# Performance work log

Measured on AMD Instinct MI355X. Metric: run time of the kernel, lower is better.

The kernel has to match this reference:

```python
import jax, jax.numpy as jnp
import numpy as np

R = 2  # decimation factor


def _cheby1_sos(N=8, rp=0.05, Wn=1.0 / R):
    """Chebyshev type-I lowpass, second-order sections (matches scipy.signal.cheby1 math)."""
    eps = np.sqrt(10.0 ** (rp / 10.0) - 1.0)
    mu = np.arcsinh(1.0 / eps) / N
    k = np.arange(1, N + 1)
    theta = np.pi * (2 * k - 1) / (2 * N)
    # analog prototype poles (no zeros)
    p = -np.sinh(mu) * np.sin(theta) + 1j * np.cosh(mu) * np.cos(theta)
    gain = np.real(np.prod(-p))
    if N % 2 == 0:
        gain /= np.sqrt(1.0 + eps * eps)
    # prewarp + lp2lp
    fs = 2.0
    warped = 2.0 * fs * np.tan(np.pi * Wn / fs)
    p = p * warped
    gain = gain * warped ** N
    # bilinear transform (zeros -> z=-1, order N)
    fs2 = 2.0 * fs
    pz = (fs2 + p) / (fs2 - p)
    gain = gain / np.real(np.prod(fs2 - p))
    # pair complex-conjugate poles into biquads (N even, all complex)
    pp = pz[np.imag(pz) > 0]
    a1 = -2.0 * np.real(pp)
    a2 = np.abs(pp) ** 2
    g = gain ** (1.0 / len(pp))  # distribute gain evenly across sections
    b0 = np.full(len(pp), g)
    sos = np.stack([b0, 2.0 * b0, b0, np.ones(len(pp)), a1, a2], axis=1)
    return sos  # [nsec, 6] float64


_SOS = _cheby1_sos()


def _sosfilt(x):
    """Cascaded biquads, direct form II transposed, zero initial state. x: [B, T]."""
    B = x.shape[0]
    nsec = _SOS.shape[0]
    b0 = jnp.asarray(_SOS[:, 0], x.dtype)
    b1 = jnp.asarray(_SOS[:, 1], x.dtype)
    b2 = jnp.asarray(_SOS[:, 2], x.dtype)
    a1 = jnp.asarray(_SOS[:, 4], x.dtype)
    a2 = jnp.asarray(_SOS[:, 5], x.dtype)

    def step(carry, xt):  # carry: (z1, z2) each [B, nsec]; xt: [B]
        z1, z2 = carry
        y = xt
        nz1, nz2 = [], []
        for s in range(nsec):  # fixed small unroll over sections
            out = b0[s] * y + z1[:, s]
            nz1.append(b1[s] * y + z2[:, s] - a1[s] * out)
            nz2.append(b2[s] * y - a2[s] * out)
            y = out
        return (jnp.stack(nz1, axis=1), jnp.stack(nz2, axis=1)), y

    z0 = jnp.zeros((B, nsec), x.dtype)
    _, ys = jax.lax.scan(step, (z0, z0), x.T)  # scan over time
    return ys.T  # [B, T]


def setup_inputs() -> dict:
    key = jax.random.key(0)
    x = jax.random.normal(key, (32, 131072), dtype=jnp.float32)
    return {"x": x}


def reference(x) -> jnp.ndarray:
    y = _sosfilt(x)
    return y[..., ::R]
```

## Files before the change

kernel.cpp:

```cpp
#include <hip/hip_runtime.h>
#include <cmath>
#include <complex>


#define T_LEN   131072
#define B_ROWS  32
#define OUT_LEN (T_LEN / 2)
#define L_CHUNK 64
#define H_WARM  128
#define TPB     256
#define BLOCKS_PER_ROW (T_LEN / (L_CHUNK * TPB))
#define WIN_FLOATS (TPB * L_CHUNK + H_WARM)
#define WIN_UNITS  (WIN_FLOATS / 4)
#define LDS_UNITS  (WIN_UNITS + 8)
#define NBLOCKS (B_ROWS * BLOCKS_PER_ROW)

struct Coef { float g; float a1[4]; float a2[4]; };

__global__ __launch_bounds__(256) void cheby_decimate_kernel(
    const float* __restrict__ x, float* __restrict__ out, Coef c)
{
    __shared__ float4 lds[LDS_UNITS];
    const int t   = threadIdx.x;
    const int row = blockIdx.x / BLOCKS_PER_ROW;
    const int bc  = blockIdx.x % BLOCKS_PER_ROW;
    const float* __restrict__ xr = x + (size_t)row * T_LEN;
    const int wstart = bc * (TPB * L_CHUNK) - H_WARM;

    #pragma unroll
    for (int k = 0; k < (WIN_UNITS + TPB - 1) / TPB; ++k) {
        int w = t + TPB * k;
        if (w < WIN_UNITS) {
            int g = wstart + 4 * w;
            float4 v = make_float4(0.f, 0.f, 0.f, 0.f);
            if (g >= 0) v = *reinterpret_cast<const float4*>(xr + g);
            lds[w ^ ((w >> 4) & 7)] = v;
        }
    }
    if (t < 8)
        lds[WIN_UNITS + t] = make_float4(0.f, 0.f, 0.f, 0.f);
    __syncthreads();

    const float g0   = c.g;
    const float na10 = -c.a1[0], na20 = -c.a2[0];
    const float na11 = -c.a1[1], na21 = -c.a2[1];
    const float na12 = -c.a1[2], na22 = -c.a2[2];
    const float na13 = -c.a1[3], na23 = -c.a2[3];

    float z11=0.f,z12=0.f, z21=0.f,z22=0.f, z31=0.f,z32=0.f, z41=0.f,z42=0.f;
    float y1=0.f, y2=0.f, y3=0.f;

#define LREAD(u) lds[(u) ^ (((u) >> 4) & 7)]
#define SEC(yin, z1, z2, na1, na2, oo) do {                                    \
        float w_ = g0 * (yin); oo = w_ + z1;                                   \
        z1 = fmaf(na1, oo, fmaf(2.f, w_, z2)); z2 = fmaf(na2, oo, w_);         \
    } while (0)
#define PSTEP(xi, STORE) do {                                                  \
        float o1, o2, o3, o4;                                                  \
        SEC((xi), z11, z12, na10, na20, o1);                                   \
        SEC(y1,   z21, z22, na11, na21, o2);                                   \
        SEC(y2,   z31, z32, na12, na22, o3);                                   \
        SEC(y3,   z41, z42, na13, na23, o4);                                   \
        y1 = o1; y2 = o2; y3 = o3; STORE;                                      \
    } while (0)

    const int ub = 16 * t;
    float4 cur = LREAD(ub);
    float outv[32];

    #pragma unroll 4
    for (int m = 0; m < 32; ++m) {
        float4 nxt = LREAD(ub + m + 1);
        PSTEP(cur.x, (void)0); PSTEP(cur.y, (void)0);
        PSTEP(cur.z, (void)0); PSTEP(cur.w, (void)0);
        cur = nxt;
    }
    #pragma unroll
    for (int m = 32; m <= 48; ++m) {
        float4 nxt = (m < 48) ? LREAD(ub + m + 1)
                              : make_float4(0.f, 0.f, 0.f, 0.f);
        PSTEP(cur.x, (void)0);
        PSTEP(cur.y, if (m >= 33) outv[2*m - 65] = o4);
        PSTEP(cur.z, (void)0);
        PSTEP(cur.w, if (m <= 47) outv[2*m - 64] = o4);
        cur = nxt;
    }
#undef PSTEP
#undef SEC
#undef LREAD

    __syncthreads();
    #pragma unroll
    for (int q = 0; q < 8; ++q) {
        lds[8*t + (q ^ (t & 7))] =
            make_float4(outv[4*q], outv[4*q+1], outv[4*q+2], outv[4*q+3]);
    }
    __syncthreads();
    const size_t obase = (size_t)row * OUT_LEN + (size_t)bc * (TPB * L_CHUNK / 2);
    #pragma unroll
    for (int k = 0; k < 8; ++k) {
        int v = t + TPB * k;
        float4 d = lds[(v & ~7) + ((v & 7) ^ ((v >> 3) & 7))];
        *reinterpret_cast<float4*>(out + obase + 4 * v) = d;
    }
}

extern "C" void kernel_launch(void* const* d_in, const int* in_sizes, int n_in,
                              void* d_out, int out_size, void* d_ws, size_t ws_size,
                              hipStream_t stream)
{
    const float* x = (const float*)d_in[0];
    float* out = (float*)d_out;

    const int N = 8;
    const double rp = 0.05;
    const double eps = std::sqrt(std::pow(10.0, rp / 10.0) - 1.0);
    const double mu  = std::asinh(1.0 / eps) / N;

    std::complex<double> p[8];
    std::complex<double> prodnp(1.0, 0.0);
    for (int i = 0; i < N; ++i) {
        double theta = M_PI * (2.0 * (i + 1) - 1.0) / (2.0 * N);
        p[i] = std::complex<double>(-std::sinh(mu) * std::sin(theta),
                                     std::cosh(mu) * std::cos(theta));
        prodnp *= -p[i];
    }
    double gain = prodnp.real() / std::sqrt(1.0 + eps * eps);

    const double fs = 2.0;
    const double warped = 2.0 * fs * std::tan(M_PI * 0.5 / fs);
    std::complex<double> prodden(1.0, 0.0);
    std::complex<double> pz[8];
    for (int i = 0; i < N; ++i) {
        p[i] *= warped;
        pz[i] = (2.0 * fs + p[i]) / (2.0 * fs - p[i]);
        prodden *= (2.0 * fs - p[i]);
    }
    gain *= std::pow(warped, (double)N);
    gain /= prodden.real();

    Coef c;
    int ns = 0;
    double A1[4], A2[4];
    for (int i = 0; i < N; ++i) {
        if (pz[i].imag() > 0.0) {
            A1[ns] = -2.0 * pz[i].real();
            A2[ns] = std::norm(pz[i]);
            ++ns;
        }
    }
    const double gsec = std::pow(gain, 1.0 / ns);
    c.g = (float)gsec;
    for (int s = 0; s < 4; ++s) { c.a1[s] = (float)A1[s]; c.a2[s] = (float)A2[s]; }

    dim3 block(TPB), grid(NBLOCKS);
    hipLaunchKernelGGL(cheby_decimate_kernel, grid, block, 0, stream, x, out, c);
}
```

Before: 71.50 us.

## Pipeline biquad cascade as two packed-float pairs and store outputs directly

```diff
diff --git a/kernel.cpp b/kernel.cpp
--- a/kernel.cpp
+++ b/kernel.cpp
@@ -14,6 +14,20 @@
 #define WIN_UNITS  (WIN_FLOATS / 4)
 #define LDS_UNITS  (WIN_UNITS + 8)
 #define NBLOCKS (B_ROWS * BLOCKS_PER_ROW)
+
+typedef float v2f __attribute__((ext_vector_type(2)));
+
+#if defined(__has_builtin)
+# if __has_builtin(__builtin_elementwise_fma)
+#  define FMA2(a, b, c) __builtin_elementwise_fma((a), (b), (c))
+# endif
+#endif
+#ifndef FMA2
+static __device__ __forceinline__ v2f fma2_(v2f a, v2f b, v2f c) {
+    v2f r; r.x = fmaf(a.x, b.x, c.x); r.y = fmaf(a.y, b.y, c.y); return r;
+}
+# define FMA2 fma2_
+#endif
 
 struct Coef { float g; float a1[4]; float a2[4]; };
 
@@ -41,27 +55,23 @@
         lds[WIN_UNITS + t] = make_float4(0.f, 0.f, 0.f, 0.f);
     __syncthreads();
 
-    const float g0   = c.g;
-    const float na10 = -c.a1[0], na20 = -c.a2[0];
-    const float na11 = -c.a1[1], na21 = -c.a2[1];
-    const float na12 = -c.a1[2], na22 = -c.a2[2];
-    const float na13 = -c.a1[3], na23 = -c.a2[3];
+    const v2f gg   = { c.g, c.g };
+    const v2f two  = { 2.f, 2.f };
+    const v2f naA1 = { -c.a1[0], -c.a1[2] }, naA2 = { -c.a2[0], -c.a2[2] };
+    const v2f naB1 = { -c.a1[1], -c.a1[3] }, naB2 = { -c.a2[1], -c.a2[3] };
 
-    float z11=0.f,z12=0.f, z21=0.f,z22=0.f, z31=0.f,z32=0.f, z41=0.f,z42=0.f;
-    float y1=0.f, y2=0.f, y3=0.f;
+    v2f zA1 = {0.f,0.f}, zA2 = {0.f,0.f}, zB1 = {0.f,0.f}, zB2 = {0.f,0.f};
+    v2f o13 = {0.f,0.f}, o24 = {0.f,0.f};
 
 #define LREAD(u) lds[(u) ^ (((u) >> 4) & 7)]
-#define SEC(yin, z1, z2, na1, na2, oo) do {                                    \
-        float w_ = g0 * (yin); oo = w_ + z1;                                   \
-        z1 = fmaf(na1, oo, fmaf(2.f, w_, z2)); z2 = fmaf(na2, oo, w_);         \
-    } while (0)
 #define PSTEP(xi, STORE) do {                                                  \
-        float o1, o2, o3, o4;                                                  \
-        SEC((xi), z11, z12, na10, na20, o1);                                   \
-        SEC(y1,   z21, z22, na11, na21, o2);                                   \
-        SEC(y2,   z31, z32, na12, na22, o3);                                   \
-        SEC(y3,   z41, z42, na13, na23, o4);                                   \
-        y1 = o1; y2 = o2; y3 = o3; STORE;                                      \
+        v2f i13; i13.x = (xi); i13.y = o24.x;                                  \
+        v2f i24 = o13;                                                         \
+        v2f wA = gg * i13; v2f oA = wA + zA1; v2f tA = FMA2(two, wA, zA2);     \
+        zA1 = FMA2(naA1, oA, tA); zA2 = FMA2(naA2, oA, wA);                    \
+        v2f wB = gg * i24; v2f oB = wB + zB1; v2f tB = FMA2(two, wB, zB2);     \
+        zB1 = FMA2(naB1, oB, tB); zB2 = FMA2(naB2, oB, wB);                    \
+        o13 = oA; o24 = oB; STORE;                                             \
     } while (0)
 
     const int ub = 16 * t;
@@ -80,28 +90,20 @@
         float4 nxt = (m < 48) ? LREAD(ub + m + 1)
                               : make_float4(0.f, 0.f, 0.f, 0.f);
         PSTEP(cur.x, (void)0);
-        PSTEP(cur.y, if (m >= 33) outv[2*m - 65] = o4);
+        PSTEP(cur.y, if (m >= 33) outv[2*m - 65] = o24.y);
         PSTEP(cur.z, (void)0);
-        PSTEP(cur.w, if (m <= 47) outv[2*m - 64] = o4);
+        PSTEP(cur.w, if (m <= 47) outv[2*m - 64] = o24.y);
         cur = nxt;
     }
 #undef PSTEP
-#undef SEC
 #undef LREAD
 
-    __syncthreads();
+    float* __restrict__ op = out + (size_t)row * OUT_LEN
+                                 + (size_t)bc * (TPB * L_CHUNK / 2) + 32 * t;
     #pragma unroll
     for (int q = 0; q < 8; ++q) {
-        lds[8*t + (q ^ (t & 7))] =
+        *reinterpret_cast<float4*>(op + 4 * q) =
             make_float4(outv[4*q], outv[4*q+1], outv[4*q+2], outv[4*q+3]);
-    }
-    __syncthreads();
-    const size_t obase = (size_t)row * OUT_LEN + (size_t)bc * (TPB * L_CHUNK / 2);
-    #pragma unroll
-    for (int k = 0; k < 8; ++k) {
-        int v = t + TPB * k;
-        float4 d = lds[(v & ~7) + ((v & 7) ^ ((v >> 3) & 7))];
-        *reinterpret_cast<float4*>(out + obase + 4 * v) = d;
     }
 }
 
```

Measured after the change: 72.06 us. No clear change (+0.8%).
